# Optimization experiments

Hardware: AMD Instinct MI355X
Metric: run time of the kernel (lower is better)

## Reference

```python
import jax, jax.numpy as jnp
import numpy as np

B, L, DIM = 8, 512, 8          # batch, seq len, raw channels (value dim D = 2*DIM = 16)
ET, HID, H = 128, 128, 2       # embed_time, hidden_size, num_heads
MAXLEN = 512
NEG = -1e9


def setup_inputs() -> dict:
    key = jax.random.key(0)
    ks = jax.random.split(key, 40)
    def n(i, shape, s=0.05):
        return jax.random.normal(ks[i], shape, jnp.float32) * s
    vals = jax.random.normal(ks[0], (B, L, DIM), jnp.float32)
    msk = (jax.random.uniform(ks[1], (B, L, DIM)) > 0.2).astype(jnp.float32)
    x = jnp.concatenate([vals, msk], -1)                      # (B, L, 2*DIM)
    time_steps = jax.random.uniform(ks[2], (B, L), jnp.float32)
    return {
        'x': x, 'time_steps': time_steps,
        # learned time embedding: Linear(1, ET-1) periodic + Linear(1,1)
        'w_per': n(3, (1, ET - 1)), 'b_per': n(4, (ET - 1,)),
        'w_lin': n(5, (1, 1)), 'b_lin': n(6, (1,)),
        # MultiTimeAttention projections
        'Wq_t': n(7, (ET, ET)), 'bq_t': n(8, (ET,)),
        'Wk_t': n(9, (ET, ET)), 'bk_t': n(10, (ET,)),
        'Wo_t': n(11, (2 * DIM * H, HID)), 'bo_t': n(12, (HID,)),
        'pos_emb': n(13, (MAXLEN + 1, HID)), 'cls_emb': n(14, (1, HID)),
        # transformer block (BERT-style post-LN encoder layer, d_ff=HID)
        'tWq': n(15, (HID, HID)), 'tbq': n(16, (HID,)),
        'tWk': n(17, (HID, HID)), 'tbk': n(18, (HID,)),
        'tWv': n(19, (HID, HID)), 'tbv': n(20, (HID,)),
        'tWo': n(21, (HID, HID)), 'tbo': n(22, (HID,)),
        'ln1_g': jnp.ones((HID,), jnp.float32), 'ln1_b': jnp.zeros((HID,), jnp.float32),
        'fW1': n(23, (HID, HID)), 'fb1': n(24, (HID,)),
        'fW2': n(25, (HID, HID)), 'fb2': n(26, (HID,)),
        'ln2_g': jnp.ones((HID,), jnp.float32), 'ln2_b': jnp.zeros((HID,), jnp.float32),
        # BertPooler
        'pW': n(27, (HID, HID)), 'pb': n(28, (HID,)),
    }


def _time_emb(tt, w_per, b_per, w_lin, b_lin):
    tt = tt[..., None]                                        # (B, L, 1)
    return jnp.concatenate([tt @ w_lin + b_lin, jnp.sin(tt @ w_per + b_per)], -1)


def _ln(x, g, b, eps=1e-5):
    m = x.mean(-1, keepdims=True)
    v = ((x - m) ** 2).mean(-1, keepdims=True)
    return (x - m) / jnp.sqrt(v + eps) * g + b


def _mta(q_emb, k_emb, value, mask, Wq, bq, Wk, bk, Wo, bo):
    # MultiTimeAttention: scores broadcast to value-channel axis, softmax over keys
    D = value.shape[-1]
    dk = ET // H
    def split(e, W, b):
        p = e @ W + b
        return p.reshape(e.shape[0], -1, H, dk).transpose(0, 2, 1, 3)
    q = split(q_emb, Wq, bq)                                  # (Bq, H, Lq, dk)
    k = split(k_emb, Wk, bk)                                  # (B,  H, Lk, dk)
    scores = jnp.matmul(q, k.swapaxes(-1, -2)) / jnp.sqrt(jnp.float32(dk))  # (B,H,Lq,Lk)
    s5 = jnp.where(mask[:, None, None, :, :] == 0, NEG, scores[..., None])  # (B,H,Lq,Lk,D)
    p = jax.nn.softmax(s5, axis=-2)
    out = jnp.einsum('bhqkd,bkd->bhqd', p, value)             # (B, H, Lq, D)
    Bv = value.shape[0]
    out = out.transpose(0, 2, 1, 3).reshape(Bv, -1, H * D)
    return out @ Wo + bo


def _tblock(x, tWq, tbq, tWk, tbk, tWv, tbv, tWo, tbo, ln1_g, ln1_b,
            fW1, fb1, fW2, fb2, ln2_g, ln2_b):
    Bq, Lq, _ = x.shape
    dk = HID // H
    def heads(W, b):
        return (x @ W + b).reshape(Bq, Lq, H, dk).transpose(0, 2, 1, 3)
    q, k, v = heads(tWq, tbq), heads(tWk, tbk), heads(tWv, tbv)
    a = jax.nn.softmax(jnp.matmul(q, k.swapaxes(-1, -2)) / jnp.sqrt(jnp.float32(dk)), -1)
    o = jnp.matmul(a, v).transpose(0, 2, 1, 3).reshape(Bq, Lq, HID) @ tWo + tbo
    x = _ln(x + o, ln1_g, ln1_b)
    f = jax.nn.relu(x @ fW1 + fb1) @ fW2 + fb2
    return _ln(x + f, ln2_g, ln2_b)


def reference(x, time_steps, w_per, b_per, w_lin, b_lin,
              Wq_t, bq_t, Wk_t, bk_t, Wo_t, bo_t, pos_emb, cls_emb,
              tWq, tbq, tWk, tbk, tWv, tbv, tWo, tbo, ln1_g, ln1_b,
              fW1, fb1, fW2, fb2, ln2_g, ln2_b, pW, pb):
    Bx = x.shape[0]
    mask_half = x[:, :, DIM:]
    mask = jnp.concatenate([mask_half, mask_half], -1)        # (B, L, 2*DIM)
    key_e = _time_emb(time_steps, w_per, b_per, w_lin, b_lin)
    tq_e = _time_emb(time_steps, w_per, b_per, w_lin, b_lin)  # query_time_steps=None -> same
    cls_t = jnp.linspace(0.0, 1.0, 128, dtype=jnp.float32)[None]
    cls_q_e = _time_emb(cls_t, w_per, b_per, w_lin, b_lin)    # (1, 128, ET)
    cls_out = _mta(cls_q_e, key_e, x, mask, Wq_t, bq_t, Wk_t, bk_t, Wo_t, bo_t)
    out = _mta(tq_e, key_e, x, mask, Wq_t, bq_t, Wk_t, bk_t, Wo_t, bo_t)
    tb = (tWq, tbq, tWk, tbk, tWv, tbv, tWo, tbo, ln1_g, ln1_b,
          fW1, fb1, fW2, fb2, ln2_g, ln2_b)
    cls_repr = jnp.broadcast_to(cls_emb[None, :, :], (Bx, 1, HID))
    # encode(cls_out, is_pooling=True), pooling='bert': no pos emb, take token 0
    h = _tblock(jnp.concatenate([cls_repr, cls_out], 1), *tb)
    cls_pooling = jnp.tanh(h[:, 0] @ pW + pb)                 # (B, HID)
    # encode(out, is_pooling=False) [pretrain path]: pos emb + transformer, drop CLS
    h2 = jnp.concatenate([cls_repr, out], 1)                  # (B, L+1, HID)
    h2 = h2 + pos_emb[:h2.shape[1]][None]
    h2 = _tblock(h2, *tb)
    last_hidden_state = h2[:, 1:]                             # (B, L, HID)
    return cls_pooling, last_hidden_state
```

## Files before the change

kernel.cpp:

```cpp
#include <hip/hip_runtime.h>
#include <hip/hip_bf16.h>
#include <math.h>


static constexpr int NM_ = 8 * 513;
static constexpr int NC_ = 8 * 129;
static constexpr int NT_ = NM_ + NC_;

using bf = __hip_bfloat16;
typedef __attribute__((ext_vector_type(8))) short bf16x8;
typedef __attribute__((ext_vector_type(4))) short bf16x4;
typedef __attribute__((ext_vector_type(4))) float floatx4;
typedef __attribute__((ext_vector_type(8))) unsigned short ushortx8;

__device__ __forceinline__ float wave_reduce_sum(float v) {
    #pragma unroll
    for (int off = 32; off >= 1; off >>= 1) v += __shfl_xor(v, off);
    return v;
}
__device__ __forceinline__ float wave_reduce_max(float v) {
    #pragma unroll
    for (int off = 32; off >= 1; off >>= 1) v = fmaxf(v, __shfl_xor(v, off));
    return v;
}
__device__ __forceinline__ float u2f(unsigned short u) {
    return __uint_as_float(((unsigned)u) << 16);
}
__device__ __forceinline__ unsigned short f2u(float f) {
    unsigned u = __float_as_uint(f);
    return (unsigned short)((u + 0x7FFF + ((u >> 16) & 1)) >> 16);
}
__device__ __forceinline__ bf16x8 join8(bf16x4 lo, bf16x4 hi) {
    return __builtin_shufflevector(lo, hi, 0, 1, 2, 3, 4, 5, 6, 7);
}
__device__ __forceinline__ float rdin(const void* p, int i, int flag) {
    return flag ? u2f(((const unsigned short*)p)[i]) : ((const float*)p)[i];
}

struct PrepAll {
    const void* src[32]; int n[32]; int dstoff[32]; int conv[32];
    const void* wsrc[8]; unsigned short* wdst[8]; float wscale[8];
    const void* ts; const void* w_per; const void* b_per;
    const void* w_lin; const void* b_lin;
    unsigned short* key_e16;
    const unsigned short* det;
};
__global__ void prep_all_kernel(PrepAll a, float* dst) {
    int flag = (a.det[0] == 0x3F80u) ? 1 : 0;
    int blk = blockIdx.x, tid = threadIdx.x;
    if (blk < 8224) {
        int which = blk / 257, bi = blk - which * 257;
        if (!a.conv[which]) return;
        int i = bi * 256 + tid;
        if (i < a.n[which]) dst[a.dstoff[which] + i] = rdin(a.src[which], i, flag);
    } else if (blk < 8736) {
        int p = blk - 8224;
        int m = p >> 6;
        int idx = (p & 63) * 256 + tid;
        int c = idx >> 9;
        int l = (idx >> 3) & 63;
        int j = idx & 7;
        int k = (c >> 3) * 32 + (l >> 4) * 8 + j;
        int n = (c & 7) * 16 + (l & 15);
        a.wdst[m][idx] = f2u(rdin(a.wsrc[m], k * 128 + n, flag) * a.wscale[m]);
    } else {
        int p = blk - 8736;
        int row = p * 2 + (tid >> 7), j = tid & 127;
        float t = (row < 4096) ? rdin(a.ts, row, flag)
                               : (float)(row - 4096) * (1.0f / 127.0f);
        float v;
        if (j == 0) v = t * rdin(a.w_lin, 0, flag) + rdin(a.b_lin, 0, flag);
        else        v = sinf(t * rdin(a.w_per, j - 1, flag) + rdin(a.b_per, j - 1, flag));
        a.key_e16[row * 128 + j] = f2u(v);
    }
}

struct GemmM {
    const void* A[3]; const unsigned short* W[3]; const float* bias[3];
    unsigned short* C[3];
    int M[3]; float bscale[3];
};
__global__ void __launch_bounds__(256)
gemm_mfma_kernel(GemmM p) {
    int y = blockIdx.y;
    const unsigned short* Wsw = p.W[y];
    const float* bias = p.bias[y];
    unsigned short* C = p.C[y];
    int M = p.M[y];
    float bscale = p.bscale[y];
    int m0 = blockIdx.x * 16;
    if (m0 >= M) return;
    __shared__ unsigned short As[16][136];
    int tid = threadIdx.x;
    {
        const unsigned short* A = (const unsigned short*)p.A[y];
        int r = tid >> 4, c0 = (tid & 15) * 8;
        ushortx8 v = {0, 0, 0, 0, 0, 0, 0, 0};
        if (m0 + r < M) v = *(const ushortx8*)(A + (size_t)(m0 + r) * 128 + c0);
        *(ushortx8*)&As[r][c0] = v;
    }
    __syncthreads();

    int wv = tid >> 6, lane = tid & 63;
    floatx4 acc0 = {0.f, 0.f, 0.f, 0.f}, acc1 = acc0;
    int am = lane & 15, aq = lane >> 4;
    #pragma unroll
    for (int ks = 0; ks < 4; ++ks) {
        bf16x8 af = *(bf16x8*)&As[am][ks * 32 + aq * 8];
        const unsigned short* base = Wsw + ((size_t)ks * 8 + 2 * wv) * 512 + lane * 8;
        bf16x8 b0 = *(const bf16x8*)(base);
        bf16x8 b1 = *(const bf16x8*)(base + 512);
        acc0 = __builtin_amdgcn_mfma_f32_16x16x32_bf16(af, b0, acc0, 0, 0, 0);
        acc1 = __builtin_amdgcn_mfma_f32_16x16x32_bf16(af, b1, acc1, 0, 0, 0);
    }
    int col = lane & 15, rowb = (lane >> 4) * 4;
    #pragma unroll
    for (int t = 0; t < 2; ++t) {
        floatx4 acc = t ? acc1 : acc0;
        int n = wv * 32 + t * 16 + col;
        float bv = bias[n] * bscale;
        #pragma unroll
        for (int rg = 0; rg < 4; ++rg) {
            int m = m0 + rowb + rg;
            if (m < M) C[(size_t)m * 128 + n] = f2u(acc[rg] + bv);
        }
    }
}

__global__ void __launch_bounds__(256)
mta_qkv_kernel(const float* att, const float* Wo, const float* bo,
               const float* cls_emb, const float* pos, float* xin,
               const unsigned short* Wq, const unsigned short* Wk, const unsigned short* Wv,
               const float* bq, const float* bk, const float* bv_,
               unsigned short* outq, unsigned short* outk, unsigned short* outv) {
    int m0 = blockIdx.x * 16;
    __shared__ float As32[16][36];
    __shared__ unsigned short As[16][136];
    int tid = threadIdx.x;
    int r = tid >> 4, g = tid & 15, c0 = g * 8;

    int R = m0 + r;
    int srow, prow;
    if (R < NM_) {
        int b = R / 513, rr = R - b * 513;
        srow = (rr == 0) ? -1 : 1024 + b * 512 + (rr - 1);
        prow = rr;
    } else {
        int mc = R - NM_;
        int b = mc / 129, rr = mc - b * 129;
        srow = (rr == 0) ? -1 : b * 128 + (rr - 1);
        prow = -1;
    }
    if (g < 2 && srow >= 0) {
        const float* src = att + (size_t)srow * 32 + g * 16;
        *(float4*)&As32[r][g * 16]      = *(const float4*)(src);
        *(float4*)&As32[r][g * 16 + 4]  = *(const float4*)(src + 4);
        *(float4*)&As32[r][g * 16 + 8]  = *(const float4*)(src + 8);
        *(float4*)&As32[r][g * 16 + 12] = *(const float4*)(src + 12);
    }
    __syncthreads();

    float acc[8];
    if (srow < 0) {
        #pragma unroll
        for (int j = 0; j < 8; ++j) acc[j] = cls_emb[c0 + j];
    } else {
        #pragma unroll
        for (int j = 0; j < 8; ++j) acc[j] = bo[c0 + j];
        #pragma unroll 8
        for (int k = 0; k < 32; ++k) {
            float a = As32[r][k];
            const float4 w0 = *(const float4*)(Wo + (size_t)k * 128 + c0);
            const float4 w1 = *(const float4*)(Wo + (size_t)k * 128 + c0 + 4);
            acc[0] = fmaf(a, w0.x, acc[0]); acc[1] = fmaf(a, w0.y, acc[1]);
            acc[2] = fmaf(a, w0.z, acc[2]); acc[3] = fmaf(a, w0.w, acc[3]);
            acc[4] = fmaf(a, w1.x, acc[4]); acc[5] = fmaf(a, w1.y, acc[5]);
            acc[6] = fmaf(a, w1.z, acc[6]); acc[7] = fmaf(a, w1.w, acc[7]);
        }
    }
    if (prow >= 0) {
        const float* pr = pos + (size_t)prow * 128 + c0;
        float4 p0 = *(const float4*)(pr);
        float4 p1 = *(const float4*)(pr + 4);
        acc[0] += p0.x; acc[1] += p0.y; acc[2] += p0.z; acc[3] += p0.w;
        acc[4] += p1.x; acc[5] += p1.y; acc[6] += p1.z; acc[7] += p1.w;
    }
    *(float4*)(xin + (size_t)R * 128 + c0) = make_float4(acc[0], acc[1], acc[2], acc[3]);
    *(float4*)(xin + (size_t)R * 128 + c0 + 4) = make_float4(acc[4], acc[5], acc[6], acc[7]);
    *(ushort4*)&As[r][c0] = make_ushort4(f2u(acc[0]), f2u(acc[1]), f2u(acc[2]), f2u(acc[3]));
    *(ushort4*)&As[r][c0 + 4] = make_ushort4(f2u(acc[4]), f2u(acc[5]), f2u(acc[6]), f2u(acc[7]));
    __syncthreads();

    int wv = tid >> 6, lane = tid & 63;
    int am = lane & 15, aq = lane >> 4;
    int col = lane & 15, rowb = (lane >> 4) * 4;
    const unsigned short* Ws[3] = {Wq, Wk, Wv};
    const float* bs[3] = {bq, bk, bv_};
    float bsc[3] = {0.125f, 1.f, 1.f};
    unsigned short* Cs[3] = {outq, outk, outv};
    #pragma unroll
    for (int y = 0; y < 3; ++y) {
        floatx4 acc0 = {0.f, 0.f, 0.f, 0.f}, acc1 = acc0;
        #pragma unroll
        for (int ks = 0; ks < 4; ++ks) {
            bf16x8 af = *(bf16x8*)&As[am][ks * 32 + aq * 8];
            const unsigned short* base = Ws[y] + ((size_t)ks * 8 + 2 * wv) * 512 + lane * 8;
            bf16x8 b0 = *(const bf16x8*)(base);
            bf16x8 b1 = *(const bf16x8*)(base + 512);
            acc0 = __builtin_amdgcn_mfma_f32_16x16x32_bf16(af, b0, acc0, 0, 0, 0);
            acc1 = __builtin_amdgcn_mfma_f32_16x16x32_bf16(af, b1, acc1, 0, 0, 0);
        }
        #pragma unroll
        for (int t = 0; t < 2; ++t) {
            floatx4 a2 = t ? acc1 : acc0;
            int n = wv * 32 + t * 16 + col;
            float bvv = bs[y][n] * bsc[y];
            #pragma unroll
            for (int rg = 0; rg < 4; ++rg)
                Cs[y][(size_t)(m0 + rowb + rg) * 128 + n] = f2u(a2[rg] + bvv);
        }
    }
}

__global__ void __launch_bounds__(256)
attnout_ffn_kernel(const unsigned short* A, const unsigned short* Wao, const float* bao,
                   const float* resid, const float* g1, const float* b1ln,
                   const unsigned short* W1, const float* fb1,
                   const unsigned short* W2, const float* fb2,
                   const float* g2, const float* b2ln,
                   const float* pW, const float* pb, float* dout) {
    int m0 = blockIdx.x * 16;
    __shared__ unsigned short As[16][136];
    __shared__ float Xs[16][128];
    __shared__ unsigned short Hs[16][136];
    __shared__ float redS[4][4][4], redQ[4][4][4];
    __shared__ float smean[16], sinv[16];
    __shared__ float x2row[128];
    __shared__ int poolb;
    int tid = threadIdx.x;
    if (tid == 0) poolb = -1;
    {
        int r = tid >> 4, c0 = (tid & 15) * 8;
        *(ushortx8*)&As[r][c0] = *(const ushortx8*)(A + (size_t)(m0 + r) * 128 + c0);
    }
    __syncthreads();

    int wv = tid >> 6, lane = tid & 63;
    int am = lane & 15, aq = lane >> 4;
    int col = lane & 15, g = lane >> 4, rowb = g * 4;

    float ov[2][4];
    {
        floatx4 acc0 = {0.f, 0.f, 0.f, 0.f}, acc1 = acc0;
        #pragma unroll
        for (int ks = 0; ks < 4; ++ks) {
            bf16x8 af = *(bf16x8*)&As[am][ks * 32 + aq * 8];
            const unsigned short* base = Wao + ((size_t)ks * 8 + 2 * wv) * 512 + lane * 8;
            bf16x8 bb0 = *(const bf16x8*)(base);
            bf16x8 bb1 = *(const bf16x8*)(base + 512);
            acc0 = __builtin_amdgcn_mfma_f32_16x16x32_bf16(af, bb0, acc0, 0, 0, 0);
            acc1 = __builtin_amdgcn_mfma_f32_16x16x32_bf16(af, bb1, acc1, 0, 0, 0);
        }
        #pragma unroll
        for (int t = 0; t < 2; ++t) {
            int n = wv * 32 + t * 16 + col;
            float bv = bao[n];
            floatx4 acc = t ? acc1 : acc0;
            #pragma unroll
            for (int rg = 0; rg < 4; ++rg)
                ov[t][rg] = acc[rg] + bv + resid[(size_t)(m0 + rowb + rg) * 128 + n];
        }
    }
    #pragma unroll
    for (int rg = 0; rg < 4; ++rg) {
        float s = ov[0][rg] + ov[1][rg];
        float q = ov[0][rg] * ov[0][rg] + ov[1][rg] * ov[1][rg];
        #pragma unroll
        for (int off = 8; off >= 1; off >>= 1) {
            s += __shfl_xor(s, off);
            q += __shfl_xor(q, off);
        }
        if ((lane & 15) == 0) { redS[wv][g][rg] = s; redQ[wv][g][rg] = q; }
    }
    __syncthreads();
    if (tid < 16) {
        int gg = tid >> 2, rg = tid & 3;
        float s = redS[0][gg][rg] + redS[1][gg][rg] + redS[2][gg][rg] + redS[3][gg][rg];
        float q = redQ[0][gg][rg] + redQ[1][gg][rg] + redQ[2][gg][rg] + redQ[3][gg][rg];
        float mean = s * 0.0078125f;
        float var = q * 0.0078125f - mean * mean;
        smean[tid] = mean;
        sinv[tid] = rsqrtf(var + 1e-5f);
    }
    __syncthreads();
    #pragma unroll
    for (int t = 0; t < 2; ++t) {
        int n = wv * 32 + t * 16 + col;
        float gm = g1[n], bb = b1ln[n];
        #pragma unroll
        for (int rg = 0; rg < 4; ++rg) {
            int row = rowb + rg;
            float val = (ov[t][rg] - smean[row]) * sinv[row] * gm + bb;
            Xs[row][n] = val;
            As[row][n] = f2u(val);
        }
    }
    __syncthreads();

    {
        floatx4 acc0 = {0.f, 0.f, 0.f, 0.f}, acc1 = acc0;
        #pragma unroll
        for (int ks = 0; ks < 4; ++ks) {
            bf16x8 af = *(bf16x8*)&As[am][ks * 32 + aq * 8];
            const unsigned short* base = W1 + ((size_t)ks * 8 + 2 * wv) * 512 + lane * 8;
            bf16x8 bb0 = *(const bf16x8*)(base);
            bf16x8 bb1 = *(const bf16x8*)(base + 512);
            acc0 = __builtin_amdgcn_mfma_f32_16x16x32_bf16(af, bb0, acc0, 0, 0, 0);
            acc1 = __builtin_amdgcn_mfma_f32_16x16x32_bf16(af, bb1, acc1, 0, 0, 0);
        }
        #pragma unroll
        for (int t = 0; t < 2; ++t) {
            int n = wv * 32 + t * 16 + col;
            float bv = fb1[n];
            floatx4 acc = t ? acc1 : acc0;
            #pragma unroll
            for (int rg = 0; rg < 4; ++rg)
                Hs[rowb + rg][n] = f2u(fmaxf(acc[rg] + bv, 0.f));
        }
    }
    __syncthreads();

    floatx4 acc0 = {0.f, 0.f, 0.f, 0.f}, acc1 = acc0;
    #pragma unroll
    for (int ks = 0; ks < 4; ++ks) {
        bf16x8 af = *(bf16x8*)&Hs[am][ks * 32 + aq * 8];
        const unsigned short* base = W2 + ((size_t)ks * 8 + 2 * wv) * 512 + lane * 8;
        bf16x8 bb0 = *(const bf16x8*)(base);
        bf16x8 bb1 = *(const bf16x8*)(base + 512);
        acc0 = __builtin_amdgcn_mfma_f32_16x16x32_bf16(af, bb0, acc0, 0, 0, 0);
        acc1 = __builtin_amdgcn_mfma_f32_16x16x32_bf16(af, bb1, acc1, 0, 0, 0);
    }
    #pragma unroll
    for (int t = 0; t < 2; ++t) {
        int n = wv * 32 + t * 16 + col;
        float bv = fb2[n];
        floatx4 acc = t ? acc1 : acc0;
        #pragma unroll
        for (int rg = 0; rg < 4; ++rg)
            ov[t][rg] = acc[rg] + bv + Xs[rowb + rg][n];
    }
    #pragma unroll
    for (int rg = 0; rg < 4; ++rg) {
        float s = ov[0][rg] + ov[1][rg];
        float q = ov[0][rg] * ov[0][rg] + ov[1][rg] * ov[1][rg];
        #pragma unroll
        for (int off = 8; off >= 1; off >>= 1) {
            s += __shfl_xor(s, off);
            q += __shfl_xor(q, off);
        }
        if ((lane & 15) == 0) { redS[wv][g][rg] = s; redQ[wv][g][rg] = q; }
    }
    __syncthreads();
    if (tid < 16) {
        int gg = tid >> 2, rg = tid & 3;
        float s = redS[0][gg][rg] + redS[1][gg][rg] + redS[2][gg][rg] + redS[3][gg][rg];
        float q = redQ[0][gg][rg] + redQ[1][gg][rg] + redQ[2][gg][rg] + redQ[3][gg][rg];
        float mean = s * 0.0078125f;
        float var = q * 0.0078125f - mean * mean;
        smean[tid] = mean;
        sinv[tid] = rsqrtf(var + 1e-5f);
    }
    __syncthreads();
    #pragma unroll
    for (int t = 0; t < 2; ++t) {
        int n = wv * 32 + t * 16 + col;
        float gm = g2[n], bb = b2ln[n];
        #pragma unroll
        for (int rg = 0; rg < 4; ++rg) {
            int row = rowb + rg;
            int m = m0 + row;
            float val = (ov[t][rg] - smean[row]) * sinv[row] * gm + bb;
            if (m < NM_) {
                int b = m / 513, r = m - b * 513;
                if (r >= 1)
                    dout[1024 + (size_t)b * 65536 + (size_t)(r - 1) * 128 + n] = val;
            } else {
                int mc = m - NM_;
                int b = mc / 129, r = mc - b * 129;
                if (r == 0) {
                    x2row[n] = val;
                    if (n == 0) poolb = b;
                }
            }
        }
    }
    __syncthreads();
    if (poolb >= 0 && tid < 128) {
        float acc = pb[tid];
        for (int k = 0; k < 128; ++k) acc = fmaf(x2row[k], pW[(size_t)k * 128 + tid], acc);
        dout[(size_t)poolb * 128 + tid] = tanhf(acc);
    }
}

__global__ void __launch_bounds__(256)
mta_att_kernel(const unsigned short* qp_cls, const unsigned short* qp_main,
               const unsigned short* kp, const float* x,
               float* att_cls, float* att_mn) {
    int is_cls = (blockIdx.x >= 32);
    int qt = is_cls ? (blockIdx.x - 32) : blockIdx.x;
    int h = blockIdx.y, b = blockIdx.z;
    int tid = threadIdx.x, lane = tid & 63, wv = tid >> 6;
    __shared__ unsigned short Qs[16][72];
    __shared__ unsigned short KV[64][72];
    __shared__ unsigned short sp[16][520];
    __shared__ unsigned short Bt[16][520];
    float* xv = (float*)&KV[0][0];
    int q0 = qt * 16;

    if (tid < 128) {
        int r = tid >> 3, c0 = (tid & 7) * 8;
        const unsigned short* qrow = is_cls ? (qp_cls + (size_t)(q0 + r) * 128 + h * 64)
                                            : (qp_main + (size_t)(b * 512 + q0 + r) * 128 + h * 64);
        *(ushortx8*)&Qs[r][c0] = *(const ushortx8*)(qrow + c0);
    }
    __syncthreads();

    bf16x8 qf0, qf1;
    {
        int m = lane & 15, g = lane >> 4;
        qf0 = *(const bf16x8*)&Qs[m][g * 8];
        qf1 = *(const bf16x8*)&Qs[m][32 + g * 8];
    }

    for (int kt = 0; kt < 8; ++kt) {
        int k0 = kt * 64;
        {
            int kk = tid >> 3, e0 = (tid & 7) * 8;
            #pragma unroll
            for (int it = 0; it < 2; ++it, kk += 32)
                *(ushortx8*)&KV[kk][e0] =
                    *(const ushortx8*)(kp + (size_t)(b * 512 + k0 + kk) * 128 + h * 64 + e0);
        }
        __syncthreads();
        int kn = lane & 15, g = lane >> 4;
        floatx4 acc = {0.f, 0.f, 0.f, 0.f};
        {
            bf16x8 b0 = *(const bf16x8*)&KV[wv * 16 + kn][g * 8];
            acc = __builtin_amdgcn_mfma_f32_16x16x32_bf16(qf0, b0, acc, 0, 0, 0);
            bf16x8 b1 = *(const bf16x8*)&KV[wv * 16 + kn][32 + g * 8];
            acc = __builtin_amdgcn_mfma_f32_16x16x32_bf16(qf1, b1, acc, 0, 0, 0);
        }
        int colk = k0 + wv * 16 + kn;
        #pragma unroll
        for (int rg = 0; rg < 4; ++rg) sp[g * 4 + rg][colk] = f2u(acc[rg]);
        __syncthreads();
    }

    for (int rr = wv; rr < 16; rr += 4) {
        float m = -1e30f;
        for (int k = lane; k < 512; k += 64) m = fmaxf(m, u2f(sp[rr][k]));
        m = wave_reduce_max(m);
        for (int k = lane; k < 512; k += 64) sp[rr][k] = f2u(expf(u2f(sp[rr][k]) - m));
    }

    for (int kt = 0; kt < 8; ++kt) {
        int k0 = kt * 64;
        __syncthreads();
        {
            int kk = tid >> 2, c0 = (tid & 3) * 4;
            float4 v = *(const float4*)(x + (size_t)(b * 512 + k0 + kk) * 16 + c0);
            xv[kk * 17 + c0] = v.x; xv[kk * 17 + c0 + 1] = v.y;
            xv[kk * 17 + c0 + 2] = v.z; xv[kk * 17 + c0 + 3] = v.w;
        }
        __syncthreads();
        {
            int c = tid & 15, k4 = (tid >> 4) * 4;
            #pragma unroll
            for (int i = 0; i < 4; ++i) {
                int k = k4 + i;
                float val = (c < 8) ? xv[k * 17 + c] * xv[k * 17 + 8 + c]
                                    : xv[k * 17 + c];
                Bt[c][k0 + k] = f2u(val);
            }
        }
    }
    __syncthreads();

    floatx4 macc = {0.f, 0.f, 0.f, 0.f};
    {
        int mq = lane & 15, g = lane >> 4;
        #pragma unroll
        for (int cc = 0; cc < 4; ++cc) {
            int koff = (wv + cc * 4) * 32;
            bf16x8 af = *(const bf16x8*)&sp[mq][koff + g * 8];
            bf16x8 bfv = *(const bf16x8*)&Bt[mq][koff + g * 8];
            macc = __builtin_amdgcn_mfma_f32_16x16x32_bf16(af, bfv, macc, 0, 0, 0);
        }
    }
    float* redC = (float*)&KV[0][0];
    float* Cfull = redC + 1024;
    #pragma unroll
    for (int rg = 0; rg < 4; ++rg) redC[(wv * 64 + lane) * 4 + rg] = macc[rg];
    __syncthreads();
    {
        int l = tid >> 2, rg = tid & 3;
        float s = redC[l * 4 + rg] + redC[(64 + l) * 4 + rg]
                + redC[(128 + l) * 4 + rg] + redC[(192 + l) * 4 + rg];
        int row = (l >> 4) * 4 + rg, c = l & 15;
        Cfull[row * 16 + c] = s;
    }
    __syncthreads();
    if (tid < 128) {
        int r = tid >> 3, c = tid & 7;
        float num = Cfull[r * 16 + c];
        float den = Cfull[r * 16 + 8 + c];
        int row = q0 + r;
        float* dst = is_cls ? (att_cls + (size_t)(b * 128 + row) * 32)
                            : (att_mn + (size_t)(b * 512 + row) * 32);
        dst[h * 16 + c] = num / den;
        dst[h * 16 + 8 + c] = 1.0f;
    }
}

__global__ void __launch_bounds__(256)
tb_att_kernel(const unsigned short* qp, const unsigned short* kp,
              const unsigned short* vp, unsigned short* outp) {
    int is_cls = (blockIdx.x >= 33);
    int qt = is_cls ? blockIdx.x - 33 : blockIdx.x;
    int h = blockIdx.y, b = blockIdx.z;
    int Lq = is_cls ? 129 : 513;
    int base = is_cls ? (4104 + b * 129) : (b * 513);
    int nkt = is_cls ? 3 : 9;
    int tid = threadIdx.x, lane = tid & 63, wv = tid >> 6;
    __shared__ unsigned short Qs[16][72];
    __shared__ unsigned short KV[64][72];
    __shared__ unsigned short sp[16][588];
    __shared__ float rinv[16];
    int q0 = qt * 16;

    if (tid < 128) {
        int r = tid >> 3, c0 = (tid & 7) * 8;
        int qr = q0 + r;
        ushortx8 v = {0, 0, 0, 0, 0, 0, 0, 0};
        if (qr < Lq) v = *(const ushortx8*)(qp + (size_t)(base + qr) * 128 + h * 64 + c0);
        *(ushortx8*)&Qs[r][c0] = v;
    }
    __syncthreads();

    bf16x8 qf0, qf1;
    {
        int m = lane & 15, g = lane >> 4;
        qf0 = *(const bf16x8*)&Qs[m][g * 8];
        qf1 = *(const bf16x8*)&Qs[m][32 + g * 8];
    }

    for (int kt = 0; kt < nkt; ++kt) {
        int k0 = kt * 64;
        {
            int kk = tid >> 3, e0 = (tid & 7) * 8;
            #pragma unroll
            for (int it = 0; it < 2; ++it, kk += 32) {
                int krow = k0 + kk;
                ushortx8 v = {0, 0, 0, 0, 0, 0, 0, 0};
                if (krow < Lq) v = *(const ushortx8*)(kp + (size_t)(base + krow) * 128 + h * 64 + e0);
                *(ushortx8*)&KV[kk][e0] = v;
            }
        }
        __syncthreads();
        int kn = lane & 15, g = lane >> 4;
        floatx4 acc = {0.f, 0.f, 0.f, 0.f};
        {
            bf16x8 b0 = *(const bf16x8*)&KV[wv * 16 + kn][g * 8];
            acc = __builtin_amdgcn_mfma_f32_16x16x32_bf16(qf0, b0, acc, 0, 0, 0);
            bf16x8 b1 = *(const bf16x8*)&KV[wv * 16 + kn][32 + g * 8];
            acc = __builtin_amdgcn_mfma_f32_16x16x32_bf16(qf1, b1, acc, 0, 0, 0);
        }
        int colk = k0 + wv * 16 + kn;
        #pragma unroll
        for (int rg = 0; rg < 4; ++rg)
            sp[g * 4 + rg][colk] = f2u((colk < Lq) ? acc[rg] : -1e30f);
        __syncthreads();
    }

    int kend = nkt * 64;
    for (int rr = wv; rr < 16; rr += 4) {
        float m = -1e30f;
        for (int k = lane; k < kend; k += 64) m = fmaxf(m, u2f(sp[rr][k]));
        m = wave_reduce_max(m);
        float sum = 0.f;
        for (int k = lane; k < kend; k += 64) {
            float e = expf(u2f(sp[rr][k]) - m);
            sp[rr][k] = f2u(e);
            sum += e;
        }
        sum = wave_reduce_sum(sum);
        if (lane == 0) rinv[rr] = 1.f / sum;
    }

    floatx4 oacc = {0.f, 0.f, 0.f, 0.f};
    for (int kt = 0; kt < nkt; ++kt) {
        int k0 = kt * 64;
        __syncthreads();
        {
            int kk = tid & 31, e0 = (tid >> 5) * 8;
            #pragma unroll
            for (int it = 0; it < 2; ++it, kk += 32) {
                int krow = k0 + kk;
                ushortx8 v = {0, 0, 0, 0, 0, 0, 0, 0};
                if (krow < Lq) v = *(const ushortx8*)(vp + (size_t)(base + krow) * 128 + h * 64 + e0);
                #pragma unroll
                for (int j = 0; j < 8; ++j) KV[e0 + j][kk] = v[j];
            }
        }
        __syncthreads();
        int dn = lane & 15, g = lane >> 4;
        #pragma unroll
        for (int c = 0; c < 2; ++c) {
            bf16x4 plo = *(const bf16x4*)&sp[lane & 15][k0 + c * 32 + g * 8];
            bf16x4 phi = *(const bf16x4*)&sp[lane & 15][k0 + c * 32 + g * 8 + 4];
            bf16x8 vf = *(const bf16x8*)&KV[wv * 16 + dn][c * 32 + g * 8];
            oacc = __builtin_amdgcn_mfma_f32_16x16x32_bf16(join8(plo, phi), vf, oacc, 0, 0, 0);
        }
    }
    int dcol = wv * 16 + (lane & 15), g = lane >> 4;
    #pragma unroll
    for (int rg = 0; rg < 4; ++rg) {
        int q = g * 4 + rg;
        int qr = q0 + q;
        if (qr < Lq)
            outp[(size_t)(base + qr) * 128 + h * 64 + dcol] = f2u(oacc[rg] * rinv[q]);
    }
}

extern "C" void kernel_launch(void* const* d_in, const int* in_sizes, int n_in,
                              void* d_out, int out_size, void* d_ws, size_t ws_size,
                              hipStream_t stream) {
    float* w = (float*)d_ws;
    size_t off = 0;
    auto alloc = [&](size_t n) {
        float* p = w + off;
        off += (n + 3) & ~(size_t)3;
        return p;
    };
    auto allocU = [&](size_t n) { return (unsigned short*)alloc((n + 1) / 2); };

    PrepAll pa{};
    int nn = n_in < 32 ? n_in : 32;
    float* fin[32];
    const int needconv[32] = {1,0,0,0,0,0, 0,1, 0,1, 1,1, 1,1, 0,1, 0,1, 0,1,
                              0,1, 1,1, 0,1, 0,1, 1,1, 1,1};
    for (int i = 0; i < nn; ++i) {
        pa.src[i] = d_in[i];
        pa.n[i] = in_sizes[i];
        fin[i] = alloc(in_sizes[i]);
        pa.dstoff[i] = (int)(fin[i] - w);
        pa.conv[i] = needconv[i];
    }
    for (int i = nn; i < 32; ++i) { pa.src[i] = nullptr; pa.n[i] = 0; pa.dstoff[i] = 0; pa.conv[i] = 0; }

    const float* x       = fin[0];
    const float* bq_t    = fin[7];
    const float* bk_t    = fin[9];
    const float* Wo_t    = fin[10]; const float* bo_t = fin[11];
    const float* pos_emb = fin[12]; const float* cls_emb = fin[13];
    const float* tbq = fin[15]; const float* tbk = fin[17]; const float* tbv = fin[19];
    const float* tbo = fin[21];
    const float* ln1_g = fin[22]; const float* ln1_b = fin[23];
    const float* fb1 = fin[25]; const float* fb2 = fin[27];
    const float* ln2_g = fin[28]; const float* ln2_b = fin[29];
    const float* pW = fin[30]; const float* pb = fin[31];

    const int widx[8] = {8, 6, 14, 16, 18, 20, 24, 26};
    unsigned short* wsw[8];
    for (int i = 0; i < 8; ++i) {
        wsw[i] = allocU(16384);
        pa.wsrc[i] = d_in[widx[i]];
        pa.wdst[i] = wsw[i];
        pa.wscale[i] = (i == 1 || i == 2) ? 0.125f : 1.0f;
    }
    pa.ts = d_in[1]; pa.w_per = d_in[2]; pa.b_per = d_in[3];
    pa.w_lin = d_in[4]; pa.b_lin = d_in[5];
    pa.det = (const unsigned short*)d_in[22];

    unsigned short* key_e16 = allocU(4224 * 128);
    unsigned short* cls_e16 = key_e16 + 4096 * 128;
    pa.key_e16 = key_e16;

    unsigned short* qp_main16 = allocU(4096 * 128);
    unsigned short* kp_main16 = allocU(4096 * 128);
    unsigned short* qp_cls16  = allocU(128 * 128);
    float* att_all = alloc(5120 * 32);
    float* att_cls = att_all;
    float* att_mn  = att_all + 1024 * 32;
    float* xin     = alloc((size_t)NT_ * 128);
    unsigned short* tbq16 = allocU((size_t)NT_ * 128);
    unsigned short* tbk16 = allocU((size_t)NT_ * 128);
    unsigned short* tbv16 = allocU((size_t)NT_ * 128);
    unsigned short* tba16 = allocU((size_t)NT_ * 128);
    (void)ws_size;

    float* outf = (float*)d_out;

    prep_all_kernel<<<10848, 256, 0, stream>>>(pa, w);

    {
        GemmM p{};
        p.A[0] = key_e16; p.W[0] = wsw[0]; p.bias[0] = bk_t; p.C[0] = kp_main16;
        p.M[0] = 4096; p.bscale[0] = 1.f;
        p.A[1] = key_e16; p.W[1] = wsw[1]; p.bias[1] = bq_t; p.C[1] = qp_main16;
        p.M[1] = 4096; p.bscale[1] = 0.125f;
        p.A[2] = cls_e16; p.W[2] = wsw[1]; p.bias[2] = bq_t; p.C[2] = qp_cls16;
        p.M[2] = 128; p.bscale[2] = 0.125f;
        gemm_mfma_kernel<<<dim3(256, 3), 256, 0, stream>>>(p);
    }

    mta_att_kernel<<<dim3(40, 2, 8), 256, 0, stream>>>(qp_cls16, qp_main16, kp_main16,
                                                       x, att_cls, att_mn);

    mta_qkv_kernel<<<321, 256, 0, stream>>>(att_all, Wo_t, bo_t, cls_emb, pos_emb, xin,
                                            wsw[2], wsw[3], wsw[4], tbq, tbk, tbv,
                                            tbq16, tbk16, tbv16);

    tb_att_kernel<<<dim3(42, 2, 8), 256, 0, stream>>>(tbq16, tbk16, tbv16, tba16);

    attnout_ffn_kernel<<<321, 256, 0, stream>>>(tba16, wsw[5], tbo, xin, ln1_g, ln1_b,
                                                wsw[6], fb1, wsw[7], fb2, ln2_g, ln2_b,
                                                pW, pb, outf);
}
```

Measured before the change: 189.1 us.

## Fuse transformer attention with out-proj/FFN and pad sequences to tile multiples

Merges the transformer-block attention kernel and the attention-output/FFN/LayerNorm kernel into one kernel per 16-row tile. This drops the intermediate attention buffer round-trip and one launch. Sequences are padded per batch (513→528, 129→144) so tiles never straddle batches. The prep kernel now launches only the blocks that actually need conversion instead of a fixed grid with early-exit blocks. In exchange, each fused block recomputes all heads' attention before its FFN, so per-block work and register/LDS pressure increase.

```diff
diff --git a/kernel.cpp b/kernel.cpp
--- a/kernel.cpp
+++ b/kernel.cpp
@@ -3,9 +3,8 @@
 #include <math.h>
 
 
-static constexpr int NM_ = 8 * 513;
-static constexpr int NC_ = 8 * 129;
-static constexpr int NT_ = NM_ + NC_;
+static constexpr int NTP_ = 5376;
+static constexpr int TILES_ = 336;
 
 using bf = __hip_bfloat16;
 typedef __attribute__((ext_vector_type(8))) short bf16x8;
@@ -38,7 +37,9 @@
 }
 
 struct PrepAll {
-    const void* src[32]; int n[32]; int dstoff[32]; int conv[32];
+    const void* src[32]; int n[32]; int dstoff[32];
+    int cstart[32]; int cnum[32];
+    int ncv;
     const void* wsrc[8]; unsigned short* wdst[8]; float wscale[8];
     const void* ts; const void* w_per; const void* b_per;
     const void* w_lin; const void* b_lin;
@@ -48,13 +49,16 @@
 __global__ void prep_all_kernel(PrepAll a, float* dst) {
     int flag = (a.det[0] == 0x3F80u) ? 1 : 0;
     int blk = blockIdx.x, tid = threadIdx.x;
-    if (blk < 8224) {
-        int which = blk / 257, bi = blk - which * 257;
-        if (!a.conv[which]) return;
+    if (blk < a.ncv) {
+        int which = -1, bi = 0;
+        #pragma unroll
+        for (int i = 0; i < 32; ++i)
+            if (blk >= a.cstart[i] && blk < a.cstart[i] + a.cnum[i]) { which = i; bi = blk - a.cstart[i]; }
+        if (which < 0) return;
         int i = bi * 256 + tid;
         if (i < a.n[which]) dst[a.dstoff[which] + i] = rdin(a.src[which], i, flag);
-    } else if (blk < 8736) {
-        int p = blk - 8224;
+    } else if (blk < a.ncv + 512) {
+        int p = blk - a.ncv;
         int m = p >> 6;
         int idx = (p & 63) * 256 + tid;
         int c = idx >> 9;
@@ -64,7 +68,7 @@
         int n = (c & 7) * 16 + (l & 15);
         a.wdst[m][idx] = f2u(rdin(a.wsrc[m], k * 128 + n, flag) * a.wscale[m]);
     } else {
-        int p = blk - 8736;
+        int p = blk - a.ncv - 512;
         int row = p * 2 + (tid >> 7), j = tid & 127;
         float t = (row < 4096) ? rdin(a.ts, row, flag)
                                : (float)(row - 4096) * (1.0f / 127.0f);
@@ -128,281 +132,6 @@
 }
 
 __global__ void __launch_bounds__(256)
-mta_qkv_kernel(const float* att, const float* Wo, const float* bo,
-               const float* cls_emb, const float* pos, float* xin,
-               const unsigned short* Wq, const unsigned short* Wk, const unsigned short* Wv,
-               const float* bq, const float* bk, const float* bv_,
-               unsigned short* outq, unsigned short* outk, unsigned short* outv) {
-    int m0 = blockIdx.x * 16;
-    __shared__ float As32[16][36];
-    __shared__ unsigned short As[16][136];
-    int tid = threadIdx.x;
-    int r = tid >> 4, g = tid & 15, c0 = g * 8;
-
-    int R = m0 + r;
-    int srow, prow;
-    if (R < NM_) {
-        int b = R / 513, rr = R - b * 513;
-        srow = (rr == 0) ? -1 : 1024 + b * 512 + (rr - 1);
-        prow = rr;
-    } else {
-        int mc = R - NM_;
-        int b = mc / 129, rr = mc - b * 129;
-        srow = (rr == 0) ? -1 : b * 128 + (rr - 1);
-        prow = -1;
-    }
-    if (g < 2 && srow >= 0) {
-        const float* src = att + (size_t)srow * 32 + g * 16;
-        *(float4*)&As32[r][g * 16]      = *(const float4*)(src);
-        *(float4*)&As32[r][g * 16 + 4]  = *(const float4*)(src + 4);
-        *(float4*)&As32[r][g * 16 + 8]  = *(const float4*)(src + 8);
-        *(float4*)&As32[r][g * 16 + 12] = *(const float4*)(src + 12);
-    }
-    __syncthreads();
-
-    float acc[8];
-    if (srow < 0) {
-        #pragma unroll
-        for (int j = 0; j < 8; ++j) acc[j] = cls_emb[c0 + j];
-    } else {
-        #pragma unroll
-        for (int j = 0; j < 8; ++j) acc[j] = bo[c0 + j];
-        #pragma unroll 8
-        for (int k = 0; k < 32; ++k) {
-            float a = As32[r][k];
-            const float4 w0 = *(const float4*)(Wo + (size_t)k * 128 + c0);
-            const float4 w1 = *(const float4*)(Wo + (size_t)k * 128 + c0 + 4);
-            acc[0] = fmaf(a, w0.x, acc[0]); acc[1] = fmaf(a, w0.y, acc[1]);
-            acc[2] = fmaf(a, w0.z, acc[2]); acc[3] = fmaf(a, w0.w, acc[3]);
-            acc[4] = fmaf(a, w1.x, acc[4]); acc[5] = fmaf(a, w1.y, acc[5]);
-            acc[6] = fmaf(a, w1.z, acc[6]); acc[7] = fmaf(a, w1.w, acc[7]);
-        }
-    }
-    if (prow >= 0) {
-        const float* pr = pos + (size_t)prow * 128 + c0;
-        float4 p0 = *(const float4*)(pr);
-        float4 p1 = *(const float4*)(pr + 4);
-        acc[0] += p0.x; acc[1] += p0.y; acc[2] += p0.z; acc[3] += p0.w;
-        acc[4] += p1.x; acc[5] += p1.y; acc[6] += p1.z; acc[7] += p1.w;
-    }
-    *(float4*)(xin + (size_t)R * 128 + c0) = make_float4(acc[0], acc[1], acc[2], acc[3]);
-    *(float4*)(xin + (size_t)R * 128 + c0 + 4) = make_float4(acc[4], acc[5], acc[6], acc[7]);
-    *(ushort4*)&As[r][c0] = make_ushort4(f2u(acc[0]), f2u(acc[1]), f2u(acc[2]), f2u(acc[3]));
-    *(ushort4*)&As[r][c0 + 4] = make_ushort4(f2u(acc[4]), f2u(acc[5]), f2u(acc[6]), f2u(acc[7]));
-    __syncthreads();
-
-    int wv = tid >> 6, lane = tid & 63;
-    int am = lane & 15, aq = lane >> 4;
-    int col = lane & 15, rowb = (lane >> 4) * 4;
-    const unsigned short* Ws[3] = {Wq, Wk, Wv};
-    const float* bs[3] = {bq, bk, bv_};
-    float bsc[3] = {0.125f, 1.f, 1.f};
-    unsigned short* Cs[3] = {outq, outk, outv};
-    #pragma unroll
-    for (int y = 0; y < 3; ++y) {
-        floatx4 acc0 = {0.f, 0.f, 0.f, 0.f}, acc1 = acc0;
-        #pragma unroll
-        for (int ks = 0; ks < 4; ++ks) {
-            bf16x8 af = *(bf16x8*)&As[am][ks * 32 + aq * 8];
-            const unsigned short* base = Ws[y] + ((size_t)ks * 8 + 2 * wv) * 512 + lane * 8;
-            bf16x8 b0 = *(const bf16x8*)(base);
-            bf16x8 b1 = *(const bf16x8*)(base + 512);
-            acc0 = __builtin_amdgcn_mfma_f32_16x16x32_bf16(af, b0, acc0, 0, 0, 0);
-            acc1 = __builtin_amdgcn_mfma_f32_16x16x32_bf16(af, b1, acc1, 0, 0, 0);
-        }
-        #pragma unroll
-        for (int t = 0; t < 2; ++t) {
-            floatx4 a2 = t ? acc1 : acc0;
-            int n = wv * 32 + t * 16 + col;
-            float bvv = bs[y][n] * bsc[y];
-            #pragma unroll
-            for (int rg = 0; rg < 4; ++rg)
-                Cs[y][(size_t)(m0 + rowb + rg) * 128 + n] = f2u(a2[rg] + bvv);
-        }
-    }
-}
-
-__global__ void __launch_bounds__(256)
-attnout_ffn_kernel(const unsigned short* A, const unsigned short* Wao, const float* bao,
-                   const float* resid, const float* g1, const float* b1ln,
-                   const unsigned short* W1, const float* fb1,
-                   const unsigned short* W2, const float* fb2,
-                   const float* g2, const float* b2ln,
-                   const float* pW, const float* pb, float* dout) {
-    int m0 = blockIdx.x * 16;
-    __shared__ unsigned short As[16][136];
-    __shared__ float Xs[16][128];
-    __shared__ unsigned short Hs[16][136];
-    __shared__ float redS[4][4][4], redQ[4][4][4];
-    __shared__ float smean[16], sinv[16];
-    __shared__ float x2row[128];
-    __shared__ int poolb;
-    int tid = threadIdx.x;
-    if (tid == 0) poolb = -1;
-    {
-        int r = tid >> 4, c0 = (tid & 15) * 8;
-        *(ushortx8*)&As[r][c0] = *(const ushortx8*)(A + (size_t)(m0 + r) * 128 + c0);
-    }
-    __syncthreads();
-
-    int wv = tid >> 6, lane = tid & 63;
-    int am = lane & 15, aq = lane >> 4;
-    int col = lane & 15, g = lane >> 4, rowb = g * 4;
-
-    float ov[2][4];
-    {
-        floatx4 acc0 = {0.f, 0.f, 0.f, 0.f}, acc1 = acc0;
-        #pragma unroll
-        for (int ks = 0; ks < 4; ++ks) {
-            bf16x8 af = *(bf16x8*)&As[am][ks * 32 + aq * 8];
-            const unsigned short* base = Wao + ((size_t)ks * 8 + 2 * wv) * 512 + lane * 8;
-            bf16x8 bb0 = *(const bf16x8*)(base);
-            bf16x8 bb1 = *(const bf16x8*)(base + 512);
-            acc0 = __builtin_amdgcn_mfma_f32_16x16x32_bf16(af, bb0, acc0, 0, 0, 0);
-            acc1 = __builtin_amdgcn_mfma_f32_16x16x32_bf16(af, bb1, acc1, 0, 0, 0);
-        }
-        #pragma unroll
-        for (int t = 0; t < 2; ++t) {
-            int n = wv * 32 + t * 16 + col;
-            float bv = bao[n];
-            floatx4 acc = t ? acc1 : acc0;
-            #pragma unroll
-            for (int rg = 0; rg < 4; ++rg)
-                ov[t][rg] = acc[rg] + bv + resid[(size_t)(m0 + rowb + rg) * 128 + n];
-        }
-    }
-    #pragma unroll
-    for (int rg = 0; rg < 4; ++rg) {
-        float s = ov[0][rg] + ov[1][rg];
-        float q = ov[0][rg] * ov[0][rg] + ov[1][rg] * ov[1][rg];
-        #pragma unroll
-        for (int off = 8; off >= 1; off >>= 1) {
-            s += __shfl_xor(s, off);
-            q += __shfl_xor(q, off);
-        }
-        if ((lane & 15) == 0) { redS[wv][g][rg] = s; redQ[wv][g][rg] = q; }
-    }
-    __syncthreads();
-    if (tid < 16) {
-        int gg = tid >> 2, rg = tid & 3;
-        float s = redS[0][gg][rg] + redS[1][gg][rg] + redS[2][gg][rg] + redS[3][gg][rg];
-        float q = redQ[0][gg][rg] + redQ[1][gg][rg] + redQ[2][gg][rg] + redQ[3][gg][rg];
-        float mean = s * 0.0078125f;
-        float var = q * 0.0078125f - mean * mean;
-        smean[tid] = mean;
-        sinv[tid] = rsqrtf(var + 1e-5f);
-    }
-    __syncthreads();
-    #pragma unroll
-    for (int t = 0; t < 2; ++t) {
-        int n = wv * 32 + t * 16 + col;
-        float gm = g1[n], bb = b1ln[n];
-        #pragma unroll
-        for (int rg = 0; rg < 4; ++rg) {
-            int row = rowb + rg;
-            float val = (ov[t][rg] - smean[row]) * sinv[row] * gm + bb;
-            Xs[row][n] = val;
-            As[row][n] = f2u(val);
-        }
-    }
-    __syncthreads();
-
-    {
-        floatx4 acc0 = {0.f, 0.f, 0.f, 0.f}, acc1 = acc0;
-        #pragma unroll
-        for (int ks = 0; ks < 4; ++ks) {
-            bf16x8 af = *(bf16x8*)&As[am][ks * 32 + aq * 8];
-            const unsigned short* base = W1 + ((size_t)ks * 8 + 2 * wv) * 512 + lane * 8;
-            bf16x8 bb0 = *(const bf16x8*)(base);
-            bf16x8 bb1 = *(const bf16x8*)(base + 512);
-            acc0 = __builtin_amdgcn_mfma_f32_16x16x32_bf16(af, bb0, acc0, 0, 0, 0);
-            acc1 = __builtin_amdgcn_mfma_f32_16x16x32_bf16(af, bb1, acc1, 0, 0, 0);
-        }
-        #pragma unroll
-        for (int t = 0; t < 2; ++t) {
-            int n = wv * 32 + t * 16 + col;
-            float bv = fb1[n];
-            floatx4 acc = t ? acc1 : acc0;
-            #pragma unroll
-            for (int rg = 0; rg < 4; ++rg)
-                Hs[rowb + rg][n] = f2u(fmaxf(acc[rg] + bv, 0.f));
-        }
-    }
-    __syncthreads();
-
-    floatx4 acc0 = {0.f, 0.f, 0.f, 0.f}, acc1 = acc0;
-    #pragma unroll
-    for (int ks = 0; ks < 4; ++ks) {
-        bf16x8 af = *(bf16x8*)&Hs[am][ks * 32 + aq * 8];
-        const unsigned short* base = W2 + ((size_t)ks * 8 + 2 * wv) * 512 + lane * 8;
-        bf16x8 bb0 = *(const bf16x8*)(base);
-        bf16x8 bb1 = *(const bf16x8*)(base + 512);
-        acc0 = __builtin_amdgcn_mfma_f32_16x16x32_bf16(af, bb0, acc0, 0, 0, 0);
-        acc1 = __builtin_amdgcn_mfma_f32_16x16x32_bf16(af, bb1, acc1, 0, 0, 0);
-    }
-    #pragma unroll
-    for (int t = 0; t < 2; ++t) {
-        int n = wv * 32 + t * 16 + col;
-        float bv = fb2[n];
-        floatx4 acc = t ? acc1 : acc0;
-        #pragma unroll
-        for (int rg = 0; rg < 4; ++rg)
-            ov[t][rg] = acc[rg] + bv + Xs[rowb + rg][n];
-    }
-    #pragma unroll
-    for (int rg = 0; rg < 4; ++rg) {
-        float s = ov[0][rg] + ov[1][rg];
-        float q = ov[0][rg] * ov[0][rg] + ov[1][rg] * ov[1][rg];
-        #pragma unroll
-        for (int off = 8; off >= 1; off >>= 1) {
-            s += __shfl_xor(s, off);
-            q += __shfl_xor(q, off);
-        }
-        if ((lane & 15) == 0) { redS[wv][g][rg] = s; redQ[wv][g][rg] = q; }
-    }
-    __syncthreads();
-    if (tid < 16) {
-        int gg = tid >> 2, rg = tid & 3;
-        float s = redS[0][gg][rg] + redS[1][gg][rg] + redS[2][gg][rg] + redS[3][gg][rg];
-        float q = redQ[0][gg][rg] + redQ[1][gg][rg] + redQ[2][gg][rg] + redQ[3][gg][rg];
-        float mean = s * 0.0078125f;
-        float var = q * 0.0078125f - mean * mean;
-        smean[tid] = mean;
-        sinv[tid] = rsqrtf(var + 1e-5f);
-    }
-    __syncthreads();
-    #pragma unroll
-    for (int t = 0; t < 2; ++t) {
-        int n = wv * 32 + t * 16 + col;
-        float gm = g2[n], bb = b2ln[n];
-        #pragma unroll
-        for (int rg = 0; rg < 4; ++rg) {
-            int row = rowb + rg;
-            int m = m0 + row;
-            float val = (ov[t][rg] - smean[row]) * sinv[row] * gm + bb;
-            if (m < NM_) {
-                int b = m / 513, r = m - b * 513;
-                if (r >= 1)
-                    dout[1024 + (size_t)b * 65536 + (size_t)(r - 1) * 128 + n] = val;
-            } else {
-                int mc = m - NM_;
-                int b = mc / 129, r = mc - b * 129;
-                if (r == 0) {
-                    x2row[n] = val;
-                    if (n == 0) poolb = b;
-                }
-            }
-        }
-    }
-    __syncthreads();
-    if (poolb >= 0 && tid < 128) {
-        float acc = pb[tid];
-        for (int k = 0; k < 128; ++k) acc = fmaf(x2row[k], pW[(size_t)k * 128 + tid], acc);
-        dout[(size_t)poolb * 128 + tid] = tanhf(acc);
-    }
-}
-
-__global__ void __launch_bounds__(256)
 mta_att_kernel(const unsigned short* qp_cls, const unsigned short* qp_main,
                const unsigned short* kp, const float* x,
                float* att_cls, float* att_mn) {
@@ -523,112 +252,375 @@
 }
 
 __global__ void __launch_bounds__(256)
-tb_att_kernel(const unsigned short* qp, const unsigned short* kp,
-              const unsigned short* vp, unsigned short* outp) {
-    int is_cls = (blockIdx.x >= 33);
-    int qt = is_cls ? blockIdx.x - 33 : blockIdx.x;
-    int h = blockIdx.y, b = blockIdx.z;
-    int Lq = is_cls ? 129 : 513;
-    int base = is_cls ? (4104 + b * 129) : (b * 513);
-    int nkt = is_cls ? 3 : 9;
+mta_qkv_kernel(const float* att, const float* Wo, const float* bo,
+               const float* cls_emb, const float* pos, float* xin,
+               const unsigned short* Wq, const unsigned short* Wk, const unsigned short* Wv,
+               const float* bq, const float* bk, const float* bv_,
+               unsigned short* outq, unsigned short* outk, unsigned short* outv) {
+    int m0 = blockIdx.x * 16;
+    __shared__ float As32[16][36];
+    __shared__ unsigned short As[16][136];
+    int tid = threadIdx.x;
+    int r = tid >> 4, g = tid & 15, c0 = g * 8;
+
+    int R = m0 + r;
+    int srow, prow, pad;
+    if (R < 4224) {
+        int b = R / 528, rr = R - b * 528;
+        pad = (rr >= 513);
+        srow = (rr == 0 || pad) ? -1 : 1024 + b * 512 + (rr - 1);
+        prow = pad ? -1 : rr;
+    } else {
+        int rc = R - 4224;
+        int b = rc / 144, rr = rc - b * 144;
+        pad = (rr >= 129);
+        srow = (rr == 0 || pad) ? -1 : b * 128 + (rr - 1);
+        prow = -1;
+    }
+    if (g < 2 && srow >= 0) {
+        const float* src = att + (size_t)srow * 32 + g * 16;
+        *(float4*)&As32[r][g * 16]      = *(const float4*)(src);
+        *(float4*)&As32[r][g * 16 + 4]  = *(const float4*)(src + 4);
+        *(float4*)&As32[r][g * 16 + 8]  = *(const float4*)(src + 8);
+        *(float4*)&As32[r][g * 16 + 12] = *(const float4*)(src + 12);
+    }
+    __syncthreads();
+
+    float acc[8];
+    if (pad) {
+        #pragma unroll
+        for (int j = 0; j < 8; ++j) acc[j] = 0.f;
+    } else if (srow < 0) {
+        #pragma unroll
+        for (int j = 0; j < 8; ++j) acc[j] = cls_emb[c0 + j];
+    } else {
+        #pragma unroll
+        for (int j = 0; j < 8; ++j) acc[j] = bo[c0 + j];
+        #pragma unroll 8
+        for (int k = 0; k < 32; ++k) {
+            float a = As32[r][k];
+            const float4 w0 = *(const float4*)(Wo + (size_t)k * 128 + c0);
+            const float4 w1 = *(const float4*)(Wo + (size_t)k * 128 + c0 + 4);
+            acc[0] = fmaf(a, w0.x, acc[0]); acc[1] = fmaf(a, w0.y, acc[1]);
+            acc[2] = fmaf(a, w0.z, acc[2]); acc[3] = fmaf(a, w0.w, acc[3]);
+            acc[4] = fmaf(a, w1.x, acc[4]); acc[5] = fmaf(a, w1.y, acc[5]);
+            acc[6] = fmaf(a, w1.z, acc[6]); acc[7] = fmaf(a, w1.w, acc[7]);
+        }
+    }
+    if (prow >= 0) {
+        const float* pr = pos + (size_t)prow * 128 + c0;
+        float4 p0 = *(const float4*)(pr);
+        float4 p1 = *(const float4*)(pr + 4);
+        acc[0] += p0.x; acc[1] += p0.y; acc[2] += p0.z; acc[3] += p0.w;
+        acc[4] += p1.x; acc[5] += p1.y; acc[6] += p1.z; acc[7] += p1.w;
+    }
+    *(float4*)(xin + (size_t)R * 128 + c0) = make_float4(acc[0], acc[1], acc[2], acc[3]);
+    *(float4*)(xin + (size_t)R * 128 + c0 + 4) = make_float4(acc[4], acc[5], acc[6], acc[7]);
+    *(ushort4*)&As[r][c0] = make_ushort4(f2u(acc[0]), f2u(acc[1]), f2u(acc[2]), f2u(acc[3]));
+    *(ushort4*)&As[r][c0 + 4] = make_ushort4(f2u(acc[4]), f2u(acc[5]), f2u(acc[6]), f2u(acc[7]));
+    __syncthreads();
+
+    int wv = tid >> 6, lane = tid & 63;
+    int am = lane & 15, aq = lane >> 4;
+    int col = lane & 15, rowb = (lane >> 4) * 4;
+    const unsigned short* Ws[3] = {Wq, Wk, Wv};
+    const float* bs[3] = {bq, bk, bv_};
+    float bsc[3] = {0.125f, 1.f, 1.f};
+    unsigned short* Cs[3] = {outq, outk, outv};
+    #pragma unroll
+    for (int y = 0; y < 3; ++y) {
+        floatx4 acc0 = {0.f, 0.f, 0.f, 0.f}, acc1 = acc0;
+        #pragma unroll
+        for (int ks = 0; ks < 4; ++ks) {
+            bf16x8 af = *(bf16x8*)&As[am][ks * 32 + aq * 8];
+            const unsigned short* base = Ws[y] + ((size_t)ks * 8 + 2 * wv) * 512 + lane * 8;
+            bf16x8 b0 = *(const bf16x8*)(base);
+            bf16x8 b1 = *(const bf16x8*)(base + 512);
+            acc0 = __builtin_amdgcn_mfma_f32_16x16x32_bf16(af, b0, acc0, 0, 0, 0);
+            acc1 = __builtin_amdgcn_mfma_f32_16x16x32_bf16(af, b1, acc1, 0, 0, 0);
+        }
+        #pragma unroll
+        for (int t = 0; t < 2; ++t) {
+            floatx4 a2 = t ? acc1 : acc0;
+            int n = wv * 32 + t * 16 + col;
+            float bvv = bs[y][n] * bsc[y];
+            #pragma unroll
+            for (int rg = 0; rg < 4; ++rg)
+                Cs[y][(size_t)(m0 + rowb + rg) * 128 + n] = f2u(a2[rg] + bvv);
+        }
+    }
+}
+
+__global__ void __launch_bounds__(256)
+tbatt_ffn_kernel(const unsigned short* qp, const unsigned short* kp,
+                 const unsigned short* vp, const unsigned short* Wao, const float* bao,
+                 const float* resid, const float* g1, const float* b1ln,
+                 const unsigned short* W1, const float* fb1,
+                 const unsigned short* W2, const float* fb2,
+                 const float* g2, const float* b2ln,
+                 const float* pW, const float* pb, float* dout) {
+    int m0 = blockIdx.x * 16;
+    int bidx, q0, Lq, base;
+    if (m0 < 4224) {
+        bidx = m0 / 528; q0 = m0 - bidx * 528; Lq = 513; base = bidx * 528;
+    } else {
+        int mc = m0 - 4224;
+        bidx = mc / 144; q0 = mc % 144; Lq = 129; base = 4224 + bidx * 144;
+    }
+    int nkt = (Lq + 63) >> 6;
     int tid = threadIdx.x, lane = tid & 63, wv = tid >> 6;
     __shared__ unsigned short Qs[16][72];
     __shared__ unsigned short KV[64][72];
     __shared__ unsigned short sp[16][588];
     __shared__ float rinv[16];
-    int q0 = qt * 16;
-
-    if (tid < 128) {
-        int r = tid >> 3, c0 = (tid & 7) * 8;
-        int qr = q0 + r;
-        ushortx8 v = {0, 0, 0, 0, 0, 0, 0, 0};
-        if (qr < Lq) v = *(const ushortx8*)(qp + (size_t)(base + qr) * 128 + h * 64 + c0);
-        *(ushortx8*)&Qs[r][c0] = v;
-    }
-    __syncthreads();
-
-    bf16x8 qf0, qf1;
+    __shared__ unsigned short As[16][136];
+    __shared__ float Xs[16][128];
+    __shared__ unsigned short Hs[16][136];
+    __shared__ float redS[4][4][4], redQ[4][4][4];
+    __shared__ float smean[16], sinv[16];
+    __shared__ float x2row[128];
+    __shared__ int poolb;
+    if (tid == 0) poolb = -1;
+
+    int am = lane & 15, aq = lane >> 4;
+    int col = lane & 15, g = lane >> 4, rowb = g * 4;
+
+    for (int h = 0; h < 2; ++h) {
+        __syncthreads();
+        if (tid < 128) {
+            int r = tid >> 3, c0 = (tid & 7) * 8;
+            *(ushortx8*)&Qs[r][c0] =
+                *(const ushortx8*)(qp + (size_t)(base + q0 + r) * 128 + h * 64 + c0);
+        }
+        __syncthreads();
+        bf16x8 qf0, qf1;
+        {
+            int m = lane & 15, gg = lane >> 4;
+            qf0 = *(const bf16x8*)&Qs[m][gg * 8];
+            qf1 = *(const bf16x8*)&Qs[m][32 + gg * 8];
+        }
+        for (int kt = 0; kt < nkt; ++kt) {
+            int k0 = kt * 64;
+            {
+                int kk = tid >> 3, e0 = (tid & 7) * 8;
+                #pragma unroll
+                for (int it = 0; it < 2; ++it, kk += 32) {
+                    int krow = k0 + kk;
+                    ushortx8 v = {0, 0, 0, 0, 0, 0, 0, 0};
+                    if (krow < Lq) v = *(const ushortx8*)(kp + (size_t)(base + krow) * 128 + h * 64 + e0);
+                    *(ushortx8*)&KV[kk][e0] = v;
+                }
+            }
+            __syncthreads();
+            int kn = lane & 15;
+            floatx4 acc = {0.f, 0.f, 0.f, 0.f};
+            {
+                bf16x8 b0 = *(const bf16x8*)&KV[wv * 16 + kn][g * 8];
+                acc = __builtin_amdgcn_mfma_f32_16x16x32_bf16(qf0, b0, acc, 0, 0, 0);
+                bf16x8 b1 = *(const bf16x8*)&KV[wv * 16 + kn][32 + g * 8];
+                acc = __builtin_amdgcn_mfma_f32_16x16x32_bf16(qf1, b1, acc, 0, 0, 0);
+            }
+            int colk = k0 + wv * 16 + kn;
+            #pragma unroll
+            for (int rg = 0; rg < 4; ++rg)
+                sp[g * 4 + rg][colk] = f2u((colk < Lq) ? acc[rg] : -1e30f);
+            __syncthreads();
+        }
+        int kend = nkt * 64;
+        for (int rr = wv; rr < 16; rr += 4) {
+            float m = -1e30f;
+            for (int k = lane; k < kend; k += 64) m = fmaxf(m, u2f(sp[rr][k]));
+            m = wave_reduce_max(m);
+            float sum = 0.f;
+            for (int k = lane; k < kend; k += 64) {
+                float e = expf(u2f(sp[rr][k]) - m);
+                sp[rr][k] = f2u(e);
+                sum += e;
+            }
+            sum = wave_reduce_sum(sum);
+            if (lane == 0) rinv[rr] = 1.f / sum;
+        }
+        floatx4 oacc = {0.f, 0.f, 0.f, 0.f};
+        for (int kt = 0; kt < nkt; ++kt) {
+            int k0 = kt * 64;
+            __syncthreads();
+            {
+                int kk = tid & 31, e0 = (tid >> 5) * 8;
+                #pragma unroll
+                for (int it = 0; it < 2; ++it, kk += 32) {
+                    int krow = k0 + kk;
+                    ushortx8 v = {0, 0, 0, 0, 0, 0, 0, 0};
+                    if (krow < Lq) v = *(const ushortx8*)(vp + (size_t)(base + krow) * 128 + h * 64 + e0);
+                    #pragma unroll
+                    for (int j = 0; j < 8; ++j) KV[e0 + j][kk] = v[j];
+                }
+            }
+            __syncthreads();
+            int dn = lane & 15;
+            #pragma unroll
+            for (int c = 0; c < 2; ++c) {
+                bf16x4 plo = *(const bf16x4*)&sp[lane & 15][k0 + c * 32 + g * 8];
+                bf16x4 phi = *(const bf16x4*)&sp[lane & 15][k0 + c * 32 + g * 8 + 4];
+                bf16x8 vf = *(const bf16x8*)&KV[wv * 16 + dn][c * 32 + g * 8];
+                oacc = __builtin_amdgcn_mfma_f32_16x16x32_bf16(join8(plo, phi), vf, oacc, 0, 0, 0);
+            }
+        }
+        int dcol = h * 64 + wv * 16 + (lane & 15);
+        #pragma unroll
+        for (int rg = 0; rg < 4; ++rg) {
+            int q = g * 4 + rg;
+            As[q][dcol] = f2u(oacc[rg] * rinv[q]);
+        }
+    }
+    __syncthreads();
+
+    float ov[2][4];
     {
-        int m = lane & 15, g = lane >> 4;
-        qf0 = *(const bf16x8*)&Qs[m][g * 8];
-        qf1 = *(const bf16x8*)&Qs[m][32 + g * 8];
-    }
-
-    for (int kt = 0; kt < nkt; ++kt) {
-        int k0 = kt * 64;
-        {
-            int kk = tid >> 3, e0 = (tid & 7) * 8;
+        floatx4 acc0 = {0.f, 0.f, 0.f, 0.f}, acc1 = acc0;
+        #pragma unroll
+        for (int ks = 0; ks < 4; ++ks) {
+            bf16x8 af = *(bf16x8*)&As[am][ks * 32 + aq * 8];
+            const unsigned short* basew = Wao + ((size_t)ks * 8 + 2 * wv) * 512 + lane * 8;
+            bf16x8 bb0 = *(const bf16x8*)(basew);
+            bf16x8 bb1 = *(const bf16x8*)(basew + 512);
+            acc0 = __builtin_amdgcn_mfma_f32_16x16x32_bf16(af, bb0, acc0, 0, 0, 0);
+            acc1 = __builtin_amdgcn_mfma_f32_16x16x32_bf16(af, bb1, acc1, 0, 0, 0);
+        }
+        #pragma unroll
+        for (int t = 0; t < 2; ++t) {
+            int n = wv * 32 + t * 16 + col;
+            float bv = bao[n];
+            floatx4 acc = t ? acc1 : acc0;
             #pragma unroll
-            for (int it = 0; it < 2; ++it, kk += 32) {
-                int krow = k0 + kk;
-                ushortx8 v = {0, 0, 0, 0, 0, 0, 0, 0};
-                if (krow < Lq) v = *(const ushortx8*)(kp + (size_t)(base + krow) * 128 + h * 64 + e0);
-                *(ushortx8*)&KV[kk][e0] = v;
+            for (int rg = 0; rg < 4; ++rg)
+                ov[t][rg] = acc[rg] + bv + resid[(size_t)(m0 + rowb + rg) * 128 + n];
+        }
+    }
+    #pragma unroll
+    for (int rg = 0; rg < 4; ++rg) {
+        float s = ov[0][rg] + ov[1][rg];
+        float q = ov[0][rg] * ov[0][rg] + ov[1][rg] * ov[1][rg];
+        #pragma unroll
+        for (int off = 8; off >= 1; off >>= 1) {
+            s += __shfl_xor(s, off);
+            q += __shfl_xor(q, off);
+        }
+        if ((lane & 15) == 0) { redS[wv][g][rg] = s; redQ[wv][g][rg] = q; }
+    }
+    __syncthreads();
+    if (tid < 16) {
+        int gg = tid >> 2, rg = tid & 3;
+        float s = redS[0][gg][rg] + redS[1][gg][rg] + redS[2][gg][rg] + redS[3][gg][rg];
+        float q = redQ[0][gg][rg] + redQ[1][gg][rg] + redQ[2][gg][rg] + redQ[3][gg][rg];
+        float mean = s * 0.0078125f;
+        float var = q * 0.0078125f - mean * mean;
+        smean[tid] = mean;
+        sinv[tid] = rsqrtf(var + 1e-5f);
+    }
+    __syncthreads();
+    #pragma unroll
+    for (int t = 0; t < 2; ++t) {
+        int n = wv * 32 + t * 16 + col;
+        float gm = g1[n], bb = b1ln[n];
+        #pragma unroll
+        for (int rg = 0; rg < 4; ++rg) {
+            int row = rowb + rg;
+            float val = (ov[t][rg] - smean[row]) * sinv[row] * gm + bb;
+            Xs[row][n] = val;
+            As[row][n] = f2u(val);
+        }
+    }
+    __syncthreads();
+
+    {
+        floatx4 acc0 = {0.f, 0.f, 0.f, 0.f}, acc1 = acc0;
+        #pragma unroll
+        for (int ks = 0; ks < 4; ++ks) {
+            bf16x8 af = *(bf16x8*)&As[am][ks * 32 + aq * 8];
+            const unsigned short* basew = W1 + ((size_t)ks * 8 + 2 * wv) * 512 + lane * 8;
+            bf16x8 bb0 = *(const bf16x8*)(basew);
+            bf16x8 bb1 = *(const bf16x8*)(basew + 512);
+            acc0 = __builtin_amdgcn_mfma_f32_16x16x32_bf16(af, bb0, acc0, 0, 0, 0);
+            acc1 = __builtin_amdgcn_mfma_f32_16x16x32_bf16(af, bb1, acc1, 0, 0, 0);
+        }
+        #pragma unroll
+        for (int t = 0; t < 2; ++t) {
+            int n = wv * 32 + t * 16 + col;
+            float bv = fb1[n];
+            floatx4 acc = t ? acc1 : acc0;
+            #pragma unroll
+            for (int rg = 0; rg < 4; ++rg)
+                Hs[rowb + rg][n] = f2u(fmaxf(acc[rg] + bv, 0.f));
+        }
+    }
+    __syncthreads();
+
+    floatx4 acc0 = {0.f, 0.f, 0.f, 0.f}, acc1 = acc0;
+    #pragma unroll
+    for (int ks = 0; ks < 4; ++ks) {
+        bf16x8 af = *(bf16x8*)&Hs[am][ks * 32 + aq * 8];
+        const unsigned short* basew = W2 + ((size_t)ks * 8 + 2 * wv) * 512 + lane * 8;
+        bf16x8 bb0 = *(const bf16x8*)(basew);
+        bf16x8 bb1 = *(const bf16x8*)(basew + 512);
+        acc0 = __builtin_amdgcn_mfma_f32_16x16x32_bf16(af, bb0, acc0, 0, 0, 0);
+        acc1 = __builtin_amdgcn_mfma_f32_16x16x32_bf16(af, bb1, acc1, 0, 0, 0);
+    }
+    #pragma unroll
+    for (int t = 0; t < 2; ++t) {
+        int n = wv * 32 + t * 16 + col;
+        float bv = fb2[n];
+        floatx4 acc = t ? acc1 : acc0;
+        #pragma unroll
+        for (int rg = 0; rg < 4; ++rg)
+            ov[t][rg] = acc[rg] + bv + Xs[rowb + rg][n];
+    }
+    #pragma unroll
+    for (int rg = 0; rg < 4; ++rg) {
+        float s = ov[0][rg] + ov[1][rg];
+        float q = ov[0][rg] * ov[0][rg] + ov[1][rg] * ov[1][rg];
+        #pragma unroll
+        for (int off = 8; off >= 1; off >>= 1) {
+            s += __shfl_xor(s, off);
+            q += __shfl_xor(q, off);
+        }
+        if ((lane & 15) == 0) { redS[wv][g][rg] = s; redQ[wv][g][rg] = q; }
+    }
+    __syncthreads();
+    if (tid < 16) {
+        int gg = tid >> 2, rg = tid & 3;
+        float s = redS[0][gg][rg] + redS[1][gg][rg] + redS[2][gg][rg] + redS[3][gg][rg];
+        float q = redQ[0][gg][rg] + redQ[1][gg][rg] + redQ[2][gg][rg] + redQ[3][gg][rg];
+        float mean = s * 0.0078125f;
+        float var = q * 0.0078125f - mean * mean;
+        smean[tid] = mean;
+        sinv[tid] = rsqrtf(var + 1e-5f);
+    }
+    __syncthreads();
+    #pragma unroll
+    for (int t = 0; t < 2; ++t) {
+        int n = wv * 32 + t * 16 + col;
+        float gm = g2[n], bb = b2ln[n];
+        #pragma unroll
+        for (int rg = 0; rg < 4; ++rg) {
+            int row = rowb + rg;
+            int rr = q0 + row;
+            float val = (ov[t][rg] - smean[row]) * sinv[row] * gm + bb;
+            if (Lq == 513) {
+                if (rr >= 1 && rr < 513)
+                    dout[1024 + (size_t)bidx * 65536 + (size_t)(rr - 1) * 128 + n] = val;
+            } else {
+                if (rr == 0) {
+                    x2row[n] = val;
+                    if (n == 0) poolb = bidx;
+                }
             }
         }
-        __syncthreads();
-        int kn = lane & 15, g = lane >> 4;
-        floatx4 acc = {0.f, 0.f, 0.f, 0.f};
-        {
-            bf16x8 b0 = *(const bf16x8*)&KV[wv * 16 + kn][g * 8];
-            acc = __builtin_amdgcn_mfma_f32_16x16x32_bf16(qf0, b0, acc, 0, 0, 0);
-            bf16x8 b1 = *(const bf16x8*)&KV[wv * 16 + kn][32 + g * 8];
-            acc = __builtin_amdgcn_mfma_f32_16x16x32_bf16(qf1, b1, acc, 0, 0, 0);
-        }
-        int colk = k0 + wv * 16 + kn;
-        #pragma unroll
-        for (int rg = 0; rg < 4; ++rg)
-            sp[g * 4 + rg][colk] = f2u((colk < Lq) ? acc[rg] : -1e30f);
-        __syncthreads();
-    }
-
-    int kend = nkt * 64;
-    for (int rr = wv; rr < 16; rr += 4) {
-        float m = -1e30f;
-        for (int k = lane; k < kend; k += 64) m = fmaxf(m, u2f(sp[rr][k]));
-        m = wave_reduce_max(m);
-        float sum = 0.f;
-        for (int k = lane; k < kend; k += 64) {
-            float e = expf(u2f(sp[rr][k]) - m);
-            sp[rr][k] = f2u(e);
-            sum += e;
-        }
-        sum = wave_reduce_sum(sum);
-        if (lane == 0) rinv[rr] = 1.f / sum;
-    }
-
-    floatx4 oacc = {0.f, 0.f, 0.f, 0.f};
-    for (int kt = 0; kt < nkt; ++kt) {
-        int k0 = kt * 64;
-        __syncthreads();
-        {
-            int kk = tid & 31, e0 = (tid >> 5) * 8;
-            #pragma unroll
-            for (int it = 0; it < 2; ++it, kk += 32) {
-                int krow = k0 + kk;
-                ushortx8 v = {0, 0, 0, 0, 0, 0, 0, 0};
-                if (krow < Lq) v = *(const ushortx8*)(vp + (size_t)(base + krow) * 128 + h * 64 + e0);
-                #pragma unroll
-                for (int j = 0; j < 8; ++j) KV[e0 + j][kk] = v[j];
-            }
-        }
-        __syncthreads();
-        int dn = lane & 15, g = lane >> 4;
-        #pragma unroll
-        for (int c = 0; c < 2; ++c) {
-            bf16x4 plo = *(const bf16x4*)&sp[lane & 15][k0 + c * 32 + g * 8];
-            bf16x4 phi = *(const bf16x4*)&sp[lane & 15][k0 + c * 32 + g * 8 + 4];
-            bf16x8 vf = *(const bf16x8*)&KV[wv * 16 + dn][c * 32 + g * 8];
-            oacc = __builtin_amdgcn_mfma_f32_16x16x32_bf16(join8(plo, phi), vf, oacc, 0, 0, 0);
-        }
-    }
-    int dcol = wv * 16 + (lane & 15), g = lane >> 4;
-    #pragma unroll
-    for (int rg = 0; rg < 4; ++rg) {
-        int q = g * 4 + rg;
-        int qr = q0 + q;
-        if (qr < Lq)
-            outp[(size_t)(base + qr) * 128 + h * 64 + dcol] = f2u(oacc[rg] * rinv[q]);
+    }
+    __syncthreads();
+    if (poolb >= 0 && tid < 128) {
+        float acc = pb[tid];
+        for (int k = 0; k < 128; ++k) acc = fmaf(x2row[k], pW[(size_t)k * 128 + tid], acc);
+        dout[(size_t)poolb * 128 + tid] = tanhf(acc);
     }
 }
 
@@ -649,14 +641,24 @@
     float* fin[32];
     const int needconv[32] = {1,0,0,0,0,0, 0,1, 0,1, 1,1, 1,1, 0,1, 0,1, 0,1,
                               0,1, 1,1, 0,1, 0,1, 1,1, 1,1};
+    int ncv = 0;
     for (int i = 0; i < nn; ++i) {
         pa.src[i] = d_in[i];
         pa.n[i] = in_sizes[i];
         fin[i] = alloc(in_sizes[i]);
         pa.dstoff[i] = (int)(fin[i] - w);
-        pa.conv[i] = needconv[i];
-    }
-    for (int i = nn; i < 32; ++i) { pa.src[i] = nullptr; pa.n[i] = 0; pa.dstoff[i] = 0; pa.conv[i] = 0; }
+        if (needconv[i]) {
+            int nb = (in_sizes[i] + 255) / 256;
+            pa.cstart[i] = ncv;
+            pa.cnum[i] = nb;
+            ncv += nb;
+        } else { pa.cstart[i] = -1; pa.cnum[i] = 0; }
+    }
+    for (int i = nn; i < 32; ++i) {
+        pa.src[i] = nullptr; pa.n[i] = 0; pa.dstoff[i] = 0;
+        pa.cstart[i] = -1; pa.cnum[i] = 0;
+    }
+    pa.ncv = ncv;
 
     const float* x       = fin[0];
     const float* bq_t    = fin[7];
@@ -692,16 +694,15 @@
     float* att_all = alloc(5120 * 32);
     float* att_cls = att_all;
     float* att_mn  = att_all + 1024 * 32;
-    float* xin     = alloc((size_t)NT_ * 128);
-    unsigned short* tbq16 = allocU((size_t)NT_ * 128);
-    unsigned short* tbk16 = allocU((size_t)NT_ * 128);
-    unsigned short* tbv16 = allocU((size_t)NT_ * 128);
-    unsigned short* tba16 = allocU((size_t)NT_ * 128);
+    float* xin     = alloc((size_t)NTP_ * 128);
+    unsigned short* tbq16 = allocU((size_t)NTP_ * 128);
+    unsigned short* tbk16 = allocU((size_t)NTP_ * 128);
+    unsigned short* tbv16 = allocU((size_t)NTP_ * 128);
     (void)ws_size;
 
     float* outf = (float*)d_out;
 
-    prep_all_kernel<<<10848, 256, 0, stream>>>(pa, w);
+    prep_all_kernel<<<ncv + 512 + 2112, 256, 0, stream>>>(pa, w);
 
     {
         GemmM p{};
@@ -717,13 +718,12 @@
     mta_att_kernel<<<dim3(40, 2, 8), 256, 0, stream>>>(qp_cls16, qp_main16, kp_main16,
                                                        x, att_cls, att_mn);
 
-    mta_qkv_kernel<<<321, 256, 0, stream>>>(att_all, Wo_t, bo_t, cls_emb, pos_emb, xin,
-                                            wsw[2], wsw[3], wsw[4], tbq, tbk, tbv,
-                                            tbq16, tbk16, tbv16);
-
-    tb_att_kernel<<<dim3(42, 2, 8), 256, 0, stream>>>(tbq16, tbk16, tbv16, tba16);
-
-    attnout_ffn_kernel<<<321, 256, 0, stream>>>(tba16, wsw[5], tbo, xin, ln1_g, ln1_b,
-                                                wsw[6], fb1, wsw[7], fb2, ln2_g, ln2_b,
-                                                pW, pb, outf);
-}
+    mta_qkv_kernel<<<TILES_, 256, 0, stream>>>(att_all, Wo_t, bo_t, cls_emb, pos_emb, xin,
+                                               wsw[2], wsw[3], wsw[4], tbq, tbk, tbv,
+                                               tbq16, tbk16, tbv16);
+
+    tbatt_ffn_kernel<<<TILES_, 256, 0, stream>>>(tbq16, tbk16, tbv16, wsw[5], tbo,
+                                                 xin, ln1_g, ln1_b,
+                                                 wsw[6], fb1, wsw[7], fb2, ln2_g, ln2_b,
+                                                 pW, pb, outf);
+}
```

Result: slower. 197.1 us (+4.2%).
